# Optimization experiments

Hardware: AMD Instinct MI355X
Metric: run time of the kernel (lower is better)

Reference implementation:

```python
import jax, jax.numpy as jnp
import numpy as np

B, T, D = 4, 4096, 1024
LN_EPS = 1e-5

def _xavier(key, shape, gain=1.0):
    fan_in, fan_out = shape[1], shape[0]
    a = gain * np.sqrt(6.0 / (fan_in + fan_out))
    return jax.random.uniform(key, shape, jnp.float32, -a, a)

def setup_inputs() -> dict:
    key = jax.random.key(0)
    kx, kg, kv, ko = jax.random.split(key, 4)
    # log_decay param init so that softplus(log_decay) == decay_init (0.01)
    log_decay = jnp.asarray(np.log(np.expm1(0.01)), jnp.float32)
    return {
        "x": jax.random.normal(kx, (B, T, D), jnp.float32),
        "ln_w": jnp.ones((D,), jnp.float32),
        "ln_b": jnp.zeros((D,), jnp.float32),
        "gate_w": _xavier(kg, (D, D)),            # torch Linear weight [out, in]
        "gate_b": jnp.zeros((D,), jnp.float32),
        "value_w": _xavier(kv, (D, D), gain=0.01),
        "value_b": jnp.zeros((D,), jnp.float32),
        "out_w": _xavier(ko, (D, D), gain=0.01),
        "out_b": jnp.zeros((D,), jnp.float32),
        "log_decay": log_decay,
    }

def reference(x, ln_w, ln_b, gate_w, gate_b, value_w, value_b, out_w, out_b, log_decay):
    # LayerNorm over last dim
    mu = jnp.mean(x, axis=-1, keepdims=True)
    var = jnp.mean(jnp.square(x - mu), axis=-1, keepdims=True)
    normed = (x - mu) * jax.lax.rsqrt(var + LN_EPS) * ln_w + ln_b
    # gate / value projections (torch Linear: y = x @ W.T + b)
    g = jax.nn.sigmoid(normed @ gate_w.T + gate_b)
    v = normed @ value_w.T + value_b
    # push-pull: cumsum(g*v) - cumsum((1-g)*v) == cumsum((2g-1)*v)
    cumsum = jnp.cumsum((2.0 * g - 1.0) * v, axis=1)
    alpha = jax.nn.softplus(log_decay)
    positions = jnp.arange(T, dtype=jnp.float32)
    decay = jnp.exp(-alpha * positions)[None, :, None]  # [1, T, 1]
    output = cumsum * decay
    return x + (output @ out_w.T + out_b)
```

## Files before the change

kernel.cpp:

```cpp
#include <hip/hip_runtime.h>
#include <hip/hip_bf16.h>

#define BB 4
#define TT 4096
#define DD 1024
#define MM (BB * TT)
#define LN_EPS 1e-5f

#define NC 64
#define CL 64

typedef __attribute__((ext_vector_type(8))) short bf16x8;
typedef __attribute__((ext_vector_type(4))) float f32x4;

__device__ __forceinline__ float bfbits2f(unsigned short h) {
    return __uint_as_float(((unsigned int)h) << 16);
}
__device__ __forceinline__ unsigned short f2bfbits(float f) {
    __hip_bfloat16 h = __float2bfloat16(f);
    return *reinterpret_cast<unsigned short*>(&h);
}
__device__ __forceinline__ unsigned int pack2(float a, float b) {
    return (unsigned int)f2bfbits(a) | ((unsigned int)f2bfbits(b) << 16);
}

__device__ __forceinline__ void async_copy16(void* lds, const void* g) {
    __builtin_amdgcn_global_load_lds(
        (const __attribute__((address_space(1))) void*)g,
        (__attribute__((address_space(3))) void*)lds,
        16, 0, 0);
}

#define RAW_BAR() asm volatile("s_barrier" ::: "memory")

__global__ __launch_bounds__(256)
void prep_kernel(const float* __restrict__ s0, const float* __restrict__ s1,
                 const float* __restrict__ s2,
                 __hip_bfloat16* __restrict__ dGV,
                 __hip_bfloat16* __restrict__ dO,
                 const float* __restrict__ x,
                 const float* __restrict__ lnw,
                 const float* __restrict__ lnb,
                 __hip_bfloat16* __restrict__ normed)
{
    if (blockIdx.x < 3072) {
        const int blk = blockIdx.x;
        const int w = blk >> 10;
        const float* src = (w == 0) ? s0 : (w == 1) ? s1 : s2;
        const size_t i = ((size_t)(blk & 1023) * 256 + threadIdx.x) * 4;
        float4 v = *(const float4*)(src + i);
        uint2 o;
        o.x = pack2(v.x, v.y);
        o.y = pack2(v.z, v.w);
        size_t di;
        if (w == 2) di = i;
        else        di = ((((i >> 10) << 1) | (size_t)w) << 10) | (i & 1023);
        __hip_bfloat16* dst = (w == 2) ? dO : dGV;
        *(uint2*)((unsigned short*)dst + di) = o;
        return;
    }
    const int wv   = threadIdx.x >> 6;
    const int lane = threadIdx.x & 63;
    const int row  = (blockIdx.x - 3072) * 4 + wv;

    const float* xr = x + (size_t)row * DD + lane * 16;
    float4 v[4];
    #pragma unroll
    for (int i = 0; i < 4; ++i) v[i] = *(const float4*)(xr + i * 4);

    float s = 0.0f, ss = 0.0f;
    #pragma unroll
    for (int i = 0; i < 4; ++i) {
        s  += (v[i].x + v[i].y) + (v[i].z + v[i].w);
        ss += fmaf(v[i].x, v[i].x, fmaf(v[i].y, v[i].y,
              fmaf(v[i].z, v[i].z, v[i].w * v[i].w)));
    }
    #pragma unroll
    for (int o = 32; o > 0; o >>= 1) {
        s  += __shfl_down(s, o);
        ss += __shfl_down(ss, o);
    }
    s  = __shfl(s, 0);
    ss = __shfl(ss, 0);

    const float mu   = s * (1.0f / DD);
    const float var  = ss * (1.0f / DD) - mu * mu;
    const float rstd = rsqrtf(var + LN_EPS);

    unsigned int res[8];
    #pragma unroll
    for (int i = 0; i < 4; ++i) {
        float4 wr = *(const float4*)(lnw + lane * 16 + i * 4);
        float4 br = *(const float4*)(lnb + lane * 16 + i * 4);
        float o0 = (v[i].x - mu) * rstd * wr.x + br.x;
        float o1 = (v[i].y - mu) * rstd * wr.y + br.y;
        float o2 = (v[i].z - mu) * rstd * wr.z + br.z;
        float o3 = (v[i].w - mu) * rstd * wr.w + br.w;
        res[i * 2]     = pack2(o0, o1);
        res[i * 2 + 1] = pack2(o2, o3);
    }
    unsigned short* op = (unsigned short*)normed + (size_t)row * DD + lane * 16;
    *(uint4*)op       = make_uint4(res[0], res[1], res[2], res[3]);
    *(uint4*)(op + 8) = make_uint4(res[4], res[5], res[6], res[7]);
}

__device__ __forceinline__ void kloop256(
    const __hip_bfloat16* __restrict__ Aglb,
    const __hip_bfloat16* __restrict__ Bglb,
    short* Ab0, short* Ab1, short* Bb0, short* Bb1,
    int m0, int n0, int tid, f32x4 acc[8][4])
{
    constexpr int BK = 64;
    constexpr int K  = DD;
    const int lane = tid & 63;
    const int wave = tid >> 6;
    const int wrow = (wave & 1) * 128;
    const int wcol = (wave >> 1) * 64;
    const int lrow = lane & 15;
    const int kgrp = lane >> 4;
    const int swz  = lrow & 7;

    const __hip_bfloat16* gA[4];
    const __hip_bfloat16* gB[4];
    #pragma unroll
    for (int r = 0; r < 4; ++r) {
        const int slot = r * 512 + tid;
        const int srow = slot >> 3;
        const int gcc  = (slot & 7) ^ (srow & 7);
        gA[r] = Aglb + (size_t)(m0 + srow) * K + gcc * 8;
        gB[r] = Bglb + (size_t)(n0 + srow) * K + gcc * 8;
    }
    auto stA = [&](short* buf, int kofs) {
        #pragma unroll
        for (int r = 0; r < 4; ++r)
            async_copy16(&buf[(r * 512 + tid) * 8], gA[r] + kofs);
    };
    auto stB = [&](short* buf, int kofs) {
        #pragma unroll
        for (int r = 0; r < 4; ++r)
            async_copy16(&buf[(r * 512 + tid) * 8], gB[r] + kofs);
    };

    stA(Ab0, 0);
    stB(Bb0, 0);
    stA(Ab1, BK);
    asm volatile("s_waitcnt vmcnt(4)" ::: "memory");
    __builtin_amdgcn_s_barrier();

    bf16x8 a[4][2], b01[2][2], b23[2][2];

    for (int it = 0; it < 8; ++it) {
        const bool sT2 = (2 * it + 2) < 16;
        const bool sT3 = (2 * it + 3) < 16;
        const int kB1 = (2 * it + 1) * BK;
        const int kT2 = (2 * it + 2) * BK;
        const int kT3 = (2 * it + 3) * BK;

        #pragma unroll
        for (int f = 0; f < 4; ++f)
            #pragma unroll
            for (int ks = 0; ks < 2; ++ks)
                a[f][ks] = *(const bf16x8*)&Ab0[(wrow + f * 16 + lrow) * BK +
                                                (((ks * 4 + kgrp) ^ swz) * 8)];
        #pragma unroll
        for (int j = 0; j < 2; ++j)
            #pragma unroll
            for (int ks = 0; ks < 2; ++ks)
                b01[j][ks] = *(const bf16x8*)&Bb0[(wcol + j * 16 + lrow) * BK +
                                                  (((ks * 4 + kgrp) ^ swz) * 8)];
        stB(Bb1, kB1);
        RAW_BAR();
        __builtin_amdgcn_s_setprio(1);
        #pragma unroll
        for (int ks = 0; ks < 2; ++ks)
            #pragma unroll
            for (int f = 0; f < 4; ++f)
                #pragma unroll
                for (int j = 0; j < 2; ++j)
                    acc[f][j] = __builtin_amdgcn_mfma_f32_16x16x32_bf16(
                        b01[j][ks], a[f][ks], acc[f][j], 0, 0, 0);
        __builtin_amdgcn_s_setprio(0);
        RAW_BAR();

        #pragma unroll
        for (int j = 0; j < 2; ++j)
            #pragma unroll
            for (int ks = 0; ks < 2; ++ks)
                b23[j][ks] = *(const bf16x8*)&Bb0[(wcol + 32 + j * 16 + lrow) * BK +
                                                  (((ks * 4 + kgrp) ^ swz) * 8)];
        RAW_BAR();
        __builtin_amdgcn_s_setprio(1);
        #pragma unroll
        for (int ks = 0; ks < 2; ++ks)
            #pragma unroll
            for (int f = 0; f < 4; ++f)
                #pragma unroll
                for (int j = 0; j < 2; ++j)
                    acc[f][2 + j] = __builtin_amdgcn_mfma_f32_16x16x32_bf16(
                        b23[j][ks], a[f][ks], acc[f][2 + j], 0, 0, 0);
        __builtin_amdgcn_s_setprio(0);
        RAW_BAR();

        #pragma unroll
        for (int f = 0; f < 4; ++f)
            #pragma unroll
            for (int ks = 0; ks < 2; ++ks)
                a[f][ks] = *(const bf16x8*)&Ab0[(wrow + 64 + f * 16 + lrow) * BK +
                                                (((ks * 4 + kgrp) ^ swz) * 8)];
        RAW_BAR();
        __builtin_amdgcn_s_setprio(1);
        #pragma unroll
        for (int ks = 0; ks < 2; ++ks)
            #pragma unroll
            for (int f = 0; f < 4; ++f)
                #pragma unroll
                for (int j = 0; j < 2; ++j)
                    acc[4 + f][j] = __builtin_amdgcn_mfma_f32_16x16x32_bf16(
                        b01[j][ks], a[f][ks], acc[4 + f][j], 0, 0, 0);
        __builtin_amdgcn_s_setprio(0);
        RAW_BAR();

        if (sT2) stA(Ab0, kT2);
        if (sT2) asm volatile("s_waitcnt vmcnt(4)" ::: "memory");
        else     asm volatile("s_waitcnt vmcnt(0)" ::: "memory");
        RAW_BAR();
        __builtin_amdgcn_s_setprio(1);
        #pragma unroll
        for (int ks = 0; ks < 2; ++ks)
            #pragma unroll
            for (int f = 0; f < 4; ++f)
                #pragma unroll
                for (int j = 0; j < 2; ++j)
                    acc[4 + f][2 + j] = __builtin_amdgcn_mfma_f32_16x16x32_bf16(
                        b23[j][ks], a[f][ks], acc[4 + f][2 + j], 0, 0, 0);
        __builtin_amdgcn_s_setprio(0);
        RAW_BAR();

        #pragma unroll
        for (int f = 0; f < 4; ++f)
            #pragma unroll
            for (int ks = 0; ks < 2; ++ks)
                a[f][ks] = *(const bf16x8*)&Ab1[(wrow + f * 16 + lrow) * BK +
                                                (((ks * 4 + kgrp) ^ swz) * 8)];
        #pragma unroll
        for (int j = 0; j < 2; ++j)
            #pragma unroll
            for (int ks = 0; ks < 2; ++ks)
                b01[j][ks] = *(const bf16x8*)&Bb1[(wcol + j * 16 + lrow) * BK +
                                                  (((ks * 4 + kgrp) ^ swz) * 8)];
        if (sT2) stB(Bb0, kT2);
        RAW_BAR();
        __builtin_amdgcn_s_setprio(1);
        #pragma unroll
        for (int ks = 0; ks < 2; ++ks)
            #pragma unroll
            for (int f = 0; f < 4; ++f)
                #pragma unroll
                for (int j = 0; j < 2; ++j)
                    acc[f][j] = __builtin_amdgcn_mfma_f32_16x16x32_bf16(
                        b01[j][ks], a[f][ks], acc[f][j], 0, 0, 0);
        __builtin_amdgcn_s_setprio(0);
        RAW_BAR();

        #pragma unroll
        for (int j = 0; j < 2; ++j)
            #pragma unroll
            for (int ks = 0; ks < 2; ++ks)
                b23[j][ks] = *(const bf16x8*)&Bb1[(wcol + 32 + j * 16 + lrow) * BK +
                                                  (((ks * 4 + kgrp) ^ swz) * 8)];
        RAW_BAR();
        __builtin_amdgcn_s_setprio(1);
        #pragma unroll
        for (int ks = 0; ks < 2; ++ks)
            #pragma unroll
            for (int f = 0; f < 4; ++f)
                #pragma unroll
                for (int j = 0; j < 2; ++j)
                    acc[f][2 + j] = __builtin_amdgcn_mfma_f32_16x16x32_bf16(
                        b23[j][ks], a[f][ks], acc[f][2 + j], 0, 0, 0);
        __builtin_amdgcn_s_setprio(0);
        RAW_BAR();

        #pragma unroll
        for (int f = 0; f < 4; ++f)
            #pragma unroll
            for (int ks = 0; ks < 2; ++ks)
                a[f][ks] = *(const bf16x8*)&Ab1[(wrow + 64 + f * 16 + lrow) * BK +
                                                (((ks * 4 + kgrp) ^ swz) * 8)];
        RAW_BAR();
        __builtin_amdgcn_s_setprio(1);
        #pragma unroll
        for (int ks = 0; ks < 2; ++ks)
            #pragma unroll
            for (int f = 0; f < 4; ++f)
                #pragma unroll
                for (int j = 0; j < 2; ++j)
                    acc[4 + f][j] = __builtin_amdgcn_mfma_f32_16x16x32_bf16(
                        b01[j][ks], a[f][ks], acc[4 + f][j], 0, 0, 0);
        __builtin_amdgcn_s_setprio(0);
        RAW_BAR();

        if (sT3) stA(Ab1, kT3);
        if (it < 7) {
            if (sT3) asm volatile("s_waitcnt vmcnt(4)" ::: "memory");
            else     asm volatile("s_waitcnt vmcnt(0)" ::: "memory");
        }
        RAW_BAR();
        __builtin_amdgcn_s_setprio(1);
        #pragma unroll
        for (int ks = 0; ks < 2; ++ks)
            #pragma unroll
            for (int f = 0; f < 4; ++f)
                #pragma unroll
                for (int j = 0; j < 2; ++j)
                    acc[4 + f][2 + j] = __builtin_amdgcn_mfma_f32_16x16x32_bf16(
                        b23[j][ks], a[f][ks], acc[4 + f][2 + j], 0, 0, 0);
        __builtin_amdgcn_s_setprio(0);
        RAW_BAR();
    }
}

__global__ __launch_bounds__(512, 2)
void dual_gemm_gate(const __hip_bfloat16* __restrict__ A,
                    const __hip_bfloat16* __restrict__ Wgv,
                    const float* __restrict__ gb,
                    const float* __restrict__ vb,
                    __hip_bfloat16* __restrict__ U,
                    float* __restrict__ Pk)
{
    __shared__ short Ab[2][256 * 64];
    __shared__ short Bb[2][256 * 64];

    const int tid = threadIdx.x;
    const int m0  = blockIdx.x * 256;
    const int n0  = blockIdx.y * 256;

    f32x4 acc[8][4] = {};
    kloop256(A, Wgv, Ab[0], Ab[1], Bb[0], Bb[1], m0, n0, tid, acc);

    const int lane = tid & 63;
    const int wave = tid >> 6;
    const int wrow = (wave & 1) * 128;
    const int wcol = (wave >> 1) * 64;
    const int lrow = lane & 15;
    const int kgrp = lane >> 4;

    const int dbase = ((n0 + wcol) >> 1) + kgrp * 2;
    float2 gb2[4], vb2[4];
    #pragma unroll
    for (int j = 0; j < 4; ++j) {
        gb2[j] = *(const float2*)(gb + dbase + j * 8);
        vb2[j] = *(const float2*)(vb + dbase + j * 8);
    }

    float psx0[4] = {}, psy0[4] = {}, psx1[4] = {}, psy1[4] = {};
    #pragma unroll
    for (int f = 0; f < 8; ++f) {
        const int m = m0 + wrow + f * 16 + lrow;
        unsigned short* urow = (unsigned short*)U + (size_t)m * DD;
        #pragma unroll
        for (int j = 0; j < 4; ++j) {
            const int db = dbase + j * 8;
            const float g0 = acc[f][j][0] + gb2[j].x;
            const float v0 = acc[f][j][1] + vb2[j].x;
            const float g1 = acc[f][j][2] + gb2[j].y;
            const float v1 = acc[f][j][3] + vb2[j].y;
            const float u0 = (2.0f / (1.0f + __expf(-g0)) - 1.0f) * v0;
            const float u1 = (2.0f / (1.0f + __expf(-g1)) - 1.0f) * v1;
            *(unsigned int*)(urow + db) = pack2(u0, u1);
            if (f < 4) { psx0[j] += u0; psy0[j] += u1; }
            else       { psx1[j] += u0; psy1[j] += u1; }
        }
    }
    #pragma unroll
    for (int j = 0; j < 4; ++j) {
        #pragma unroll
        for (int mk = 1; mk <= 8; mk <<= 1) {
            psx0[j] += __shfl_xor(psx0[j], mk);
            psy0[j] += __shfl_xor(psy0[j], mk);
            psx1[j] += __shfl_xor(psx1[j], mk);
            psy1[j] += __shfl_xor(psy1[j], mk);
        }
    }
    if (lrow == 0) {
        const int grow = m0 + wrow;
        const int cb   = grow >> 12;
        const int cc   = (grow & (TT - 1)) >> 6;
        #pragma unroll
        for (int j = 0; j < 4; ++j) {
            const int db = dbase + j * 8;
            *(float2*)&Pk[((size_t)cb * NC + cc) * DD + db] =
                make_float2(psx0[j], psy0[j]);
            *(float2*)&Pk[((size_t)cb * NC + cc + 1) * DD + db] =
                make_float2(psx1[j], psy1[j]);
        }
    }
}

__global__ __launch_bounds__(512, 2)
void gemm_out(const __hip_bfloat16* __restrict__ S,
              const __hip_bfloat16* __restrict__ Wo,
              const float* __restrict__ bias,
              const float* __restrict__ X,
              float* __restrict__ C)
{
    __shared__ short Ab[2][256 * 64];
    __shared__ short Bb[2][256 * 64];

    const int tid = threadIdx.x;
    const int m0  = blockIdx.x * 256;
    const int n0  = blockIdx.y * 256;

    f32x4 acc[8][4] = {};
    kloop256(S, Wo, Ab[0], Ab[1], Bb[0], Bb[1], m0, n0, tid, acc);

    const int lane = tid & 63;
    const int wave = tid >> 6;
    const int wrow = (wave & 1) * 128;
    const int wcol = (wave >> 1) * 64;
    const int lrow = lane & 15;
    const int kgrp = lane >> 4;

    float4 bv[4];
    #pragma unroll
    for (int j = 0; j < 4; ++j)
        bv[j] = *(const float4*)(bias + n0 + wcol + j * 16 + kgrp * 4);

    #pragma unroll
    for (int f = 0; f < 8; ++f) {
        const int m = m0 + wrow + f * 16 + lrow;
        #pragma unroll
        for (int j = 0; j < 4; ++j) {
            const int nb = n0 + wcol + j * 16 + kgrp * 4;
            const size_t idx = (size_t)m * DD + nb;
            const float4 xv = *(const float4*)(X + idx);
            float4 o;
            o.x = acc[f][j][0] + bv[j].x + xv.x;
            o.y = acc[f][j][1] + bv[j].y + xv.y;
            o.z = acc[f][j][2] + bv[j].z + xv.z;
            o.w = acc[f][j][3] + bv[j].w + xv.w;
            *(float4*)(C + idx) = o;
        }
    }
}

__global__ __launch_bounds__(1024)
void scan_final(const __hip_bfloat16* __restrict__ U,
                const float* __restrict__ Pk,
                const float* __restrict__ log_decay,
                __hip_bfloat16* __restrict__ S)
{
    __shared__ float LdsC[8][DD];
    __shared__ float LdsP[8][DD];

    const int c  = blockIdx.x, b = blockIdx.y;
    const int w  = threadIdx.x >> 7;
    const int dg = threadIdx.x & 127;
    const int d8 = dg * 8;

    const float ld    = log_decay[0];
    const float alpha = log1pf(__expf(ld));
    const float ratio = __expf(-alpha);

    const size_t base = ((size_t)b * TT + (size_t)c * CL + w * 8) * DD + d8;
    const unsigned short* up = (const unsigned short*)U + base;

    uint4 raw[8];
    float cs[8] = {0.f, 0.f, 0.f, 0.f, 0.f, 0.f, 0.f, 0.f};
    #pragma unroll
    for (int r = 0; r < 8; ++r) {
        raw[r] = *(const uint4*)(up + (size_t)r * DD);
        const unsigned int wds[4] = {raw[r].x, raw[r].y, raw[r].z, raw[r].w};
        #pragma unroll
        for (int k = 0; k < 4; ++k) {
            cs[2 * k]     += bfbits2f((unsigned short)(wds[k] & 0xFFFF));
            cs[2 * k + 1] += bfbits2f((unsigned short)(wds[k] >> 16));
        }
    }

    float pp[8] = {0.f, 0.f, 0.f, 0.f, 0.f, 0.f, 0.f, 0.f};
    for (int cc = w; cc < c; cc += 8) {
        const float* pr = &Pk[((size_t)b * NC + cc) * DD + d8];
        const float4 a0 = *(const float4*)pr;
        const float4 a1 = *(const float4*)(pr + 4);
        pp[0] += a0.x; pp[1] += a0.y; pp[2] += a0.z; pp[3] += a0.w;
        pp[4] += a1.x; pp[5] += a1.y; pp[6] += a1.z; pp[7] += a1.w;
    }

    *(float4*)&LdsC[w][d8]     = make_float4(cs[0], cs[1], cs[2], cs[3]);
    *(float4*)&LdsC[w][d8 + 4] = make_float4(cs[4], cs[5], cs[6], cs[7]);
    *(float4*)&LdsP[w][d8]     = make_float4(pp[0], pp[1], pp[2], pp[3]);
    *(float4*)&LdsP[w][d8 + 4] = make_float4(pp[4], pp[5], pp[6], pp[7]);
    __syncthreads();

    float run[8] = {0.f, 0.f, 0.f, 0.f, 0.f, 0.f, 0.f, 0.f};
    #pragma unroll
    for (int w2 = 0; w2 < 8; ++w2) {
        const float4 p0 = *(const float4*)&LdsP[w2][d8];
        const float4 p1 = *(const float4*)&LdsP[w2][d8 + 4];
        run[0] += p0.x; run[1] += p0.y; run[2] += p0.z; run[3] += p0.w;
        run[4] += p1.x; run[5] += p1.y; run[6] += p1.z; run[7] += p1.w;
        if (w2 < w) {
            const float4 c0 = *(const float4*)&LdsC[w2][d8];
            const float4 c1 = *(const float4*)&LdsC[w2][d8 + 4];
            run[0] += c0.x; run[1] += c0.y; run[2] += c0.z; run[3] += c0.w;
            run[4] += c1.x; run[5] += c1.y; run[6] += c1.z; run[7] += c1.w;
        }
    }

    float dec = __expf(-alpha * (float)(c * CL + w * 8));
    unsigned short* sp = (unsigned short*)S + base;
    #pragma unroll
    for (int r = 0; r < 8; ++r) {
        const unsigned int wds[4] = {raw[r].x, raw[r].y, raw[r].z, raw[r].w};
        uint4 o;
        unsigned int* ow = (unsigned int*)&o;
        #pragma unroll
        for (int k = 0; k < 4; ++k) {
            run[2 * k]     += bfbits2f((unsigned short)(wds[k] & 0xFFFF));
            run[2 * k + 1] += bfbits2f((unsigned short)(wds[k] >> 16));
            ow[k] = pack2(run[2 * k] * dec, run[2 * k + 1] * dec);
        }
        *(uint4*)(sp + (size_t)r * DD) = o;
        dec *= ratio;
    }
}

extern "C" void kernel_launch(void* const* d_in, const int* in_sizes, int n_in,
                              void* d_out, int out_size, void* d_ws, size_t ws_size,
                              hipStream_t stream)
{
    const float* x        = (const float*)d_in[0];
    const float* ln_w     = (const float*)d_in[1];
    const float* ln_b     = (const float*)d_in[2];
    const float* gate_w   = (const float*)d_in[3];
    const float* gate_b   = (const float*)d_in[4];
    const float* value_w  = (const float*)d_in[5];
    const float* value_b  = (const float*)d_in[6];
    const float* out_w    = (const float*)d_in[7];
    const float* out_b    = (const float*)d_in[8];
    const float* log_dec  = (const float*)d_in[9];
    float* out = (float*)d_out;

    char* ws = (char*)d_ws;
    const size_t MB = 1024 * 1024;
    __hip_bfloat16* normed = (__hip_bfloat16*)(ws);
    __hip_bfloat16* S      = (__hip_bfloat16*)(ws);
    float*          Pk     = (float*)(ws + 32 * MB);
    __hip_bfloat16* Wgv16  = (__hip_bfloat16*)(ws + 33 * MB);
    __hip_bfloat16* Wo16   = (__hip_bfloat16*)(ws + 37 * MB);
    __hip_bfloat16* U      = (__hip_bfloat16*)d_out;

    prep_kernel<<<dim3(3072 + MM / 4), dim3(256), 0, stream>>>(
        gate_w, value_w, out_w, Wgv16, Wo16, x, ln_w, ln_b, normed);

    dual_gemm_gate<<<dim3(MM / 256, 2048 / 256), dim3(512), 0, stream>>>(
        normed, Wgv16, gate_b, value_b, U, Pk);

    scan_final<<<dim3(NC, BB), dim3(1024), 0, stream>>>(U, Pk, log_dec, S);

    gemm_out<<<dim3(MM / 256, DD / 256), dim3(512), 0, stream>>>(
        S, Wo16, out_b, x, out);
}
```

Before: 266.6 us.

## Replace interleaved gate/value GEMM with separate-weight 128x128 dual-accumulator kernel

Measured after the change: 272.7 us. 2.3% more time.

```diff
diff --git a/kernel.cpp b/kernel.cpp
--- a/kernel.cpp
+++ b/kernel.cpp
@@ -36,8 +36,8 @@
 __global__ __launch_bounds__(256)
 void prep_kernel(const float* __restrict__ s0, const float* __restrict__ s1,
                  const float* __restrict__ s2,
-                 __hip_bfloat16* __restrict__ dGV,
-                 __hip_bfloat16* __restrict__ dO,
+                 __hip_bfloat16* __restrict__ d0, __hip_bfloat16* __restrict__ d1,
+                 __hip_bfloat16* __restrict__ d2,
                  const float* __restrict__ x,
                  const float* __restrict__ lnw,
                  const float* __restrict__ lnb,
@@ -47,16 +47,13 @@
         const int blk = blockIdx.x;
         const int w = blk >> 10;
         const float* src = (w == 0) ? s0 : (w == 1) ? s1 : s2;
+        __hip_bfloat16* dst = (w == 0) ? d0 : (w == 1) ? d1 : d2;
         const size_t i = ((size_t)(blk & 1023) * 256 + threadIdx.x) * 4;
         float4 v = *(const float4*)(src + i);
         uint2 o;
         o.x = pack2(v.x, v.y);
         o.y = pack2(v.z, v.w);
-        size_t di;
-        if (w == 2) di = i;
-        else        di = ((((i >> 10) << 1) | (size_t)w) << 10) | (i & 1023);
-        __hip_bfloat16* dst = (w == 2) ? dO : dGV;
-        *(uint2*)((unsigned short*)dst + di) = o;
+        *(uint2*)((unsigned short*)dst + i) = o;
         return;
     }
     const int wv   = threadIdx.x >> 6;
@@ -102,6 +99,122 @@
     unsigned short* op = (unsigned short*)normed + (size_t)row * DD + lane * 16;
     *(uint4*)op       = make_uint4(res[0], res[1], res[2], res[3]);
     *(uint4*)(op + 8) = make_uint4(res[4], res[5], res[6], res[7]);
+}
+
+__global__ __launch_bounds__(256, 2)
+void dual_gemm_gate(const __hip_bfloat16* __restrict__ A,
+                    const __hip_bfloat16* __restrict__ Wg,
+                    const __hip_bfloat16* __restrict__ Wv,
+                    const float* __restrict__ gb,
+                    const float* __restrict__ vb,
+                    __hip_bfloat16* __restrict__ U,
+                    float* __restrict__ Pk,
+                    int M, int N, int K)
+{
+    constexpr int BK = 64;
+    __shared__ short As[128 * BK];
+    __shared__ short Bg[128 * BK];
+    __shared__ short Bv[128 * BK];
+
+    const int tid  = threadIdx.x;
+    const int m0   = blockIdx.x * 128;
+    const int n0   = blockIdx.y * 128;
+    const int wave = tid >> 6;
+    const int lane = tid & 63;
+    const int wm   = (wave & 1) * 64;
+    const int wn   = (wave >> 1) * 64;
+    const int lrow = lane & 15;
+    const int kgrp = lane >> 4;
+    const int swz  = lrow & 7;
+
+    f32x4 accg[4][4] = {};
+    f32x4 accv[4][4] = {};
+
+    const __hip_bfloat16* gA[4];
+    const __hip_bfloat16* gG[4];
+    const __hip_bfloat16* gV[4];
+    #pragma unroll
+    for (int r = 0; r < 4; ++r) {
+        const int slot = r * 256 + tid;
+        const int srow = slot >> 3;
+        const int gcc  = (slot & 7) ^ (srow & 7);
+        gA[r] = A  + (size_t)(m0 + srow) * K + gcc * 8;
+        gG[r] = Wg + (size_t)(n0 + srow) * K + gcc * 8;
+        gV[r] = Wv + (size_t)(n0 + srow) * K + gcc * 8;
+    }
+
+    for (int k0 = 0; k0 < K; k0 += BK) {
+        #pragma unroll
+        for (int r = 0; r < 4; ++r) {
+            async_copy16(&As[(r * 256 + tid) * 8], gA[r] + k0);
+            async_copy16(&Bg[(r * 256 + tid) * 8], gG[r] + k0);
+            async_copy16(&Bv[(r * 256 + tid) * 8], gV[r] + k0);
+        }
+        __builtin_amdgcn_s_waitcnt(0);
+        __syncthreads();
+
+        #pragma unroll
+        for (int ks = 0; ks < 2; ++ks) {
+            const int co = ((ks * 4 + kgrp) ^ swz) * 8;
+            bf16x8 af[4], bgf[4], bvf[4];
+            #pragma unroll
+            for (int i = 0; i < 4; ++i)
+                af[i] = *(const bf16x8*)&As[(wm + i * 16 + lrow) * BK + co];
+            #pragma unroll
+            for (int j = 0; j < 4; ++j) {
+                bgf[j] = *(const bf16x8*)&Bg[(wn + j * 16 + lrow) * BK + co];
+                bvf[j] = *(const bf16x8*)&Bv[(wn + j * 16 + lrow) * BK + co];
+            }
+            #pragma unroll
+            for (int i = 0; i < 4; ++i)
+                #pragma unroll
+                for (int j = 0; j < 4; ++j) {
+                    accg[i][j] = __builtin_amdgcn_mfma_f32_16x16x32_bf16(
+                        bgf[j], af[i], accg[i][j], 0, 0, 0);
+                    accv[i][j] = __builtin_amdgcn_mfma_f32_16x16x32_bf16(
+                        bvf[j], af[i], accv[i][j], 0, 0, 0);
+                }
+        }
+        __syncthreads();
+    }
+
+    const int chrow = m0 + wm;
+    const int cb    = chrow >> 12;
+    const int cc    = (chrow & (TT - 1)) >> 6;
+
+    #pragma unroll
+    for (int j = 0; j < 4; ++j) {
+        const int nb = n0 + wn + j * 16 + kgrp * 4;
+        const float4 gb4 = *(const float4*)(gb + nb);
+        const float4 vb4 = *(const float4*)(vb + nb);
+        float4 ps = make_float4(0.f, 0.f, 0.f, 0.f);
+        #pragma unroll
+        for (int i = 0; i < 4; ++i) {
+            const int m = m0 + wm + i * 16 + lrow;
+            const float g0 = accg[i][j][0] + gb4.x, v0 = accv[i][j][0] + vb4.x;
+            const float g1 = accg[i][j][1] + gb4.y, v1 = accv[i][j][1] + vb4.y;
+            const float g2 = accg[i][j][2] + gb4.z, v2 = accv[i][j][2] + vb4.z;
+            const float g3 = accg[i][j][3] + gb4.w, v3 = accv[i][j][3] + vb4.w;
+            const float u0 = (2.0f / (1.0f + __expf(-g0)) - 1.0f) * v0;
+            const float u1 = (2.0f / (1.0f + __expf(-g1)) - 1.0f) * v1;
+            const float u2 = (2.0f / (1.0f + __expf(-g2)) - 1.0f) * v2;
+            const float u3 = (2.0f / (1.0f + __expf(-g3)) - 1.0f) * v3;
+            ps.x += u0; ps.y += u1; ps.z += u2; ps.w += u3;
+            uint2 o;
+            o.x = pack2(u0, u1);
+            o.y = pack2(u2, u3);
+            *(uint2*)((unsigned short*)U + (size_t)m * N + nb) = o;
+        }
+        #pragma unroll
+        for (int mk = 1; mk <= 8; mk <<= 1) {
+            ps.x += __shfl_xor(ps.x, mk);
+            ps.y += __shfl_xor(ps.y, mk);
+            ps.z += __shfl_xor(ps.z, mk);
+            ps.w += __shfl_xor(ps.w, mk);
+        }
+        if (lrow == 0)
+            *(float4*)&Pk[((size_t)cb * NC + cc) * DD + nb] = ps;
+    }
 }
 
 __device__ __forceinline__ void kloop256(
@@ -321,83 +434,6 @@
 }
 
 __global__ __launch_bounds__(512, 2)
-void dual_gemm_gate(const __hip_bfloat16* __restrict__ A,
-                    const __hip_bfloat16* __restrict__ Wgv,
-                    const float* __restrict__ gb,
-                    const float* __restrict__ vb,
-                    __hip_bfloat16* __restrict__ U,
-                    float* __restrict__ Pk)
-{
-    __shared__ short Ab[2][256 * 64];
-    __shared__ short Bb[2][256 * 64];
-
-    const int tid = threadIdx.x;
-    const int m0  = blockIdx.x * 256;
-    const int n0  = blockIdx.y * 256;
-
-    f32x4 acc[8][4] = {};
-    kloop256(A, Wgv, Ab[0], Ab[1], Bb[0], Bb[1], m0, n0, tid, acc);
-
-    const int lane = tid & 63;
-    const int wave = tid >> 6;
-    const int wrow = (wave & 1) * 128;
-    const int wcol = (wave >> 1) * 64;
-    const int lrow = lane & 15;
-    const int kgrp = lane >> 4;
-
-    const int dbase = ((n0 + wcol) >> 1) + kgrp * 2;
-    float2 gb2[4], vb2[4];
-    #pragma unroll
-    for (int j = 0; j < 4; ++j) {
-        gb2[j] = *(const float2*)(gb + dbase + j * 8);
-        vb2[j] = *(const float2*)(vb + dbase + j * 8);
-    }
-
-    float psx0[4] = {}, psy0[4] = {}, psx1[4] = {}, psy1[4] = {};
-    #pragma unroll
-    for (int f = 0; f < 8; ++f) {
-        const int m = m0 + wrow + f * 16 + lrow;
-        unsigned short* urow = (unsigned short*)U + (size_t)m * DD;
-        #pragma unroll
-        for (int j = 0; j < 4; ++j) {
-            const int db = dbase + j * 8;
-            const float g0 = acc[f][j][0] + gb2[j].x;
-            const float v0 = acc[f][j][1] + vb2[j].x;
-            const float g1 = acc[f][j][2] + gb2[j].y;
-            const float v1 = acc[f][j][3] + vb2[j].y;
-            const float u0 = (2.0f / (1.0f + __expf(-g0)) - 1.0f) * v0;
-            const float u1 = (2.0f / (1.0f + __expf(-g1)) - 1.0f) * v1;
-            *(unsigned int*)(urow + db) = pack2(u0, u1);
-            if (f < 4) { psx0[j] += u0; psy0[j] += u1; }
-            else       { psx1[j] += u0; psy1[j] += u1; }
-        }
-    }
-    #pragma unroll
-    for (int j = 0; j < 4; ++j) {
-        #pragma unroll
-        for (int mk = 1; mk <= 8; mk <<= 1) {
-            psx0[j] += __shfl_xor(psx0[j], mk);
-            psy0[j] += __shfl_xor(psy0[j], mk);
-            psx1[j] += __shfl_xor(psx1[j], mk);
-            psy1[j] += __shfl_xor(psy1[j], mk);
-        }
-    }
-    if (lrow == 0) {
-        const int grow = m0 + wrow;
-        const int cb   = grow >> 12;
-        const int cc   = (grow & (TT - 1)) >> 6;
-        #pragma unroll
-        for (int j = 0; j < 4; ++j) {
-            const int db = dbase + j * 8;
-            *(float2*)&Pk[((size_t)cb * NC + cc) * DD + db] =
-                make_float2(psx0[j], psy0[j]);
-            *(float2*)&Pk[((size_t)cb * NC + cc + 1) * DD + db] =
-                make_float2(psx1[j], psy1[j]);
-        }
-    }
-}
-
-__global__ __launch_bounds__(512, 2)
 void gemm_out(const __hip_bfloat16* __restrict__ S,
               const __hip_bfloat16* __restrict__ Wo,
               const float* __restrict__ bias,
@@ -547,15 +583,16 @@
     __hip_bfloat16* normed = (__hip_bfloat16*)(ws);
     __hip_bfloat16* S      = (__hip_bfloat16*)(ws);
     float*          Pk     = (float*)(ws + 32 * MB);
-    __hip_bfloat16* Wgv16  = (__hip_bfloat16*)(ws + 33 * MB);
+    __hip_bfloat16* Wg16   = (__hip_bfloat16*)(ws + 33 * MB);
+    __hip_bfloat16* Wv16   = (__hip_bfloat16*)(ws + 35 * MB);
     __hip_bfloat16* Wo16   = (__hip_bfloat16*)(ws + 37 * MB);
     __hip_bfloat16* U      = (__hip_bfloat16*)d_out;
 
     prep_kernel<<<dim3(3072 + MM / 4), dim3(256), 0, stream>>>(
-        gate_w, value_w, out_w, Wgv16, Wo16, x, ln_w, ln_b, normed);
-
-    dual_gemm_gate<<<dim3(MM / 256, 2048 / 256), dim3(512), 0, stream>>>(
-        normed, Wgv16, gate_b, value_b, U, Pk);
+        gate_w, value_w, out_w, Wg16, Wv16, Wo16, x, ln_w, ln_b, normed);
+
+    dual_gemm_gate<<<dim3(MM / 128, DD / 128), dim3(256), 0, stream>>>(
+        normed, Wg16, Wv16, gate_b, value_b, U, Pk, MM, DD, DD);
 
     scan_final<<<dim3(NC, BB), dim3(1024), 0, stream>>>(U, Pk, log_dec, S);
 
```
